# Kernel tuning notes

Hardware: AMD Instinct MI355X
Metric: run time of the kernel (lower is better)

## Reference

```python
import jax, jax.numpy as jnp
import numpy as np

N_NODES = 100000


def _degree_norms(src, dst, n):
    ones = jnp.ones(src.shape[0], dtype=jnp.float32)
    deg_out = jax.ops.segment_sum(ones, src, num_segments=n)
    deg_in = jax.ops.segment_sum(ones, dst, num_segments=n)
    norm_src = jnp.where(deg_out > 0, jax.lax.rsqrt(jnp.maximum(deg_out, 1.0)), 0.0)
    norm_dst = jnp.where(deg_in > 0, jax.lax.rsqrt(jnp.maximum(deg_in, 1.0)), 0.0)
    return norm_src, norm_dst


def _gcn_layer(x, W, b, src, dst, norm_src, norm_dst, n):
    # DGL GraphConv norm='both': D_dst^{-1/2} A D_src^{-1/2} X W + b
    h = (x * norm_src[:, None]) @ W          # [N, d_out]
    agg = jax.ops.segment_sum(h[src], dst, num_segments=n)  # SpMM gather/scatter
    return agg * norm_dst[:, None] + b


def setup_inputs() -> dict:
    key = jax.random.key(0)
    ks = jax.random.split(key, 8)
    E = 1600000
    x = jax.random.normal(ks[0], (N_NODES, 128), dtype=jnp.float32)
    edge_index = jax.random.randint(ks[1], (2, E), 0, N_NODES, dtype=jnp.int64)
    s = 1.0 / np.sqrt(128.0)
    W1 = jax.random.uniform(ks[2], (128, 128), jnp.float32, -s, s)
    b1 = jnp.zeros((128,), jnp.float32)
    W2 = jax.random.uniform(ks[3], (128, 128), jnp.float32, -s, s)
    b2 = jnp.zeros((128,), jnp.float32)
    W3 = jax.random.uniform(ks[4], (128, 256), jnp.float32, -s, s)
    b3 = jnp.zeros((256,), jnp.float32)
    return {"x": x, "edge_index": edge_index, "W1": W1, "b1": b1,
            "W2": W2, "b2": b2, "W3": W3, "b3": b3}


def reference(x, edge_index, W1, b1, W2, b2, W3, b3):
    src, dst = edge_index[0], edge_index[1]
    norm_src, norm_dst = _degree_norms(src, dst, N_NODES)
    h = jax.nn.relu(_gcn_layer(x, W1, b1, src, dst, norm_src, norm_dst, N_NODES))
    h = jax.nn.relu(_gcn_layer(h, W2, b2, src, dst, norm_src, norm_dst, N_NODES))
    h = _gcn_layer(h, W3, b3, src, dst, norm_src, norm_dst, N_NODES)
    return (h, edge_index)
```

## Files before the change

kernel.cpp:

```cpp
#include <hip/hip_runtime.h>

typedef _Float16 f16;
typedef _Float16 f16x8 __attribute__((ext_vector_type(8)));
typedef float f32x2 __attribute__((ext_vector_type(2)));
typedef float f32x4 __attribute__((ext_vector_type(4)));
typedef int i32x4 __attribute__((ext_vector_type(4)));

#define ROWB 1024
#define OFF_AGG 0
#define OFF_SA 256
#define OFF_SB 384
#define OFF_ADJ 768

__device__ __forceinline__ float bf2f(unsigned short h) {
  return __uint_as_float(((unsigned)h) << 16);
}
__device__ __forceinline__ unsigned short f2bf(float f) {
  unsigned u = __float_as_uint(f);
  u += 0x7fffu + ((u >> 16) & 1u);
  return (unsigned short)(u >> 16);
}
__device__ __forceinline__ float scrub(float v) {
  if (!(v == v)) return 0.f;
  return fminf(fmaxf(v, -65504.f), 65504.f);
}
__device__ __forceinline__ float scrub8(float v) {
  if (!(v == v)) return 0.f;
  return fminf(fmaxf(v, -240.f), 240.f);
}
__device__ __forceinline__ int iclamp(int v, int lo, int hi) {
  return v < lo ? lo : (v > hi ? hi : v);
}
__device__ __forceinline__ int adj_read(const char* H, int i) {
  return *(const int*)(H + ((size_t)(i >> 6)) * ROWB + OFF_ADJ + (i & 63) * 4);
}
__device__ __forceinline__ void adj_write(char* H, int i, int v) {
  *(int*)(H + ((size_t)(i >> 6)) * ROWB + OFF_ADJ + (i & 63) * 4) = v;
}
__device__ __forceinline__ int cread(const char* H, size_t base, int i) {
  return *(const int*)(H + base + ((size_t)(i >> 7)) * ROWB + (i & 127) * 4);
}
__device__ __forceinline__ i32x4 cread4(const char* H, size_t base, int i) {
  return *(const i32x4*)(H + base + ((size_t)(i >> 7)) * ROWB + (i & 127) * 4);
}
__device__ __forceinline__ void cwrite(char* H, size_t base, int i, int v) {
  *(int*)(H + base + ((size_t)(i >> 7)) * ROWB + (i & 127) * 4) = v;
}
__device__ __forceinline__ int2 pread(const char* H, size_t base, int i) {
  return *(const int2*)(H + base + ((size_t)(i >> 6)) * ROWB + (i & 63) * 8);
}
__device__ __forceinline__ void pwrite(char* H, size_t base, int i, int2 v) {
  *(int2*)(H + base + ((size_t)(i >> 6)) * ROWB + (i & 63) * 8) = v;
}
__device__ __forceinline__ int enc4(float a, float b, float c, float d) {
  int w = __builtin_amdgcn_cvt_pk_fp8_f32(a, b, 0, false);
  w = __builtin_amdgcn_cvt_pk_fp8_f32(c, d, w, true);
  return w;
}
__device__ __forceinline__ void dec_acc(i32x4 w, float* acc, float sc) {
#pragma unroll
  for (int d = 0; d < 4; ++d) {
    f32x2 lo = __builtin_amdgcn_cvt_pk_f32_fp8(w[d], false);
    f32x2 hi = __builtin_amdgcn_cvt_pk_f32_fp8(w[d], true);
    acc[d * 4 + 0] += sc * lo[0];
    acc[d * 4 + 1] += sc * lo[1];
    acc[d * 4 + 2] += sc * hi[0];
    acc[d * 4 + 3] += sc * hi[1];
  }
}

__global__ __launch_bounds__(64) void k_detect(const int* __restrict__ ei,
                                               int* __restrict__ flag) {
  int lane = threadIdx.x;
  int v = ei[2 * lane + 1];
  unsigned long long m = __ballot(v == 0);
  if (lane == 0) *flag = (m == 0xFFFFFFFFFFFFFFFFull) ? 1 : 0;
}

__global__ __launch_bounds__(256) void k_compact(const int* __restrict__ ei, int E,
                                                 int n, const int* __restrict__ flag,
                                                 char* __restrict__ H, size_t srcB,
                                                 size_t dstB, float* __restrict__ eout) {
  const int sh = *flag;
  const int tid = threadIdx.x;
  const int base = blockIdx.x * 1024 + tid;
  const int m = 2 * E;
#pragma unroll
  for (int k = 0; k < 4; ++k) {
    int i = base + k * 256;
    if (i < m) {
      int v = ei[(size_t)i << sh];
      eout[i] = bf2f(f2bf((float)v));
      int c = iclamp(v, 0, n - 1);
      if (i < E) cwrite(H, srcB, i, c);
      else cwrite(H, dstB, i - E, c);
    }
  }
}

__global__ __launch_bounds__(256) void k_coarse(char* __restrict__ H, size_t dstB,
                                                size_t cB, int E, int R, int CE) {
  __shared__ unsigned c[64];
  const int tid = threadIdx.x;
  if (tid < 64) c[tid] = 0;
  __syncthreads();
  const int lo = blockIdx.x * CE, hi = min(lo + CE, E);
  for (int i = lo + tid; i < hi; i += 256) {
    unsigned d = (unsigned)cread(H, dstB, i);
    atomicAdd(&c[d / (unsigned)R], 1u);
  }
  __syncthreads();
  if (tid < 64) cwrite(H, cB, tid * 256 + (int)blockIdx.x, (int)c[tid]);
}

__global__ __launch_bounds__(1024) void k_cscan(char* __restrict__ H, size_t cB) {
  __shared__ int bs[1024];
  const int tid = threadIdx.x;
  const int per = 16;
  const int base = tid * per;
  int vals[16];
  int sum = 0;
#pragma unroll
  for (int j = 0; j < per; ++j) {
    vals[j] = cread(H, cB, base + j);
    sum += vals[j];
  }
  bs[tid] = sum;
  __syncthreads();
  for (int off = 1; off < 1024; off <<= 1) {
    int t = (tid >= off) ? bs[tid - off] : 0;
    __syncthreads();
    bs[tid] += t;
    __syncthreads();
  }
  int ex = bs[tid] - sum;
#pragma unroll
  for (int j = 0; j < per; ++j) {
    int v = vals[j];
    cwrite(H, cB, base + j, ex);
    ex += v;
  }
}

__global__ __launch_bounds__(256) void k_bucket(char* __restrict__ H, size_t srcB,
                                                size_t dstB, size_t cB, size_t pB,
                                                int E, int R, int CE) {
  __shared__ int cu[64];
  const int tid = threadIdx.x;
  if (tid < 64) cu[tid] = cread(H, cB, tid * 256 + (int)blockIdx.x);
  __syncthreads();
  const int lo = blockIdx.x * CE, hi = min(lo + CE, E);
  for (int i = lo + tid; i < hi; i += 256) {
    int s = cread(H, srcB, i);
    int d = cread(H, dstB, i);
    int pos = atomicAdd(&cu[(unsigned)d / (unsigned)R], 1);
    pwrite(H, pB, pos, make_int2(s, d));
  }
}

__global__ __launch_bounds__(512) void k_hsrc(char* __restrict__ H, size_t srcB,
                                              size_t poB, int NPAD, int n, int E, int R) {
  extern __shared__ unsigned hh[];
  const int r = blockIdx.x >> 2, sl = blockIdx.x & 3;
  const int lo = r * R;
  if (lo >= n) return;
  const int hi = min(lo + R, n);
  const int tid = threadIdx.x;
  for (int j = tid; j < R; j += 512) hh[j] = 0;
  __syncthreads();
  int ES = (((E + 3) / 4) + 3) & ~3;
  const int s0 = sl * ES, s1 = min(s0 + ES, E);
  const int span = (unsigned)(hi - lo);
  const int m4 = s0 + ((s1 - s0) & ~3);
  for (int i = s0 + tid * 4; i < m4; i += 2048) {
    i32x4 v = cread4(H, srcB, i);
#pragma unroll
    for (int k = 0; k < 4; ++k) {
      unsigned u = (unsigned)(v[k] - lo);
      if (u < (unsigned)span) atomicAdd(&hh[u], 1u);
    }
  }
  for (int i = m4 + tid; i < s1; i += 512) {
    unsigned u = (unsigned)(cread(H, srcB, i) - lo);
    if (u < (unsigned)span) atomicAdd(&hh[u], 1u);
  }
  __syncthreads();
  for (int j = tid; j < hi - lo; j += 512) cwrite(H, poB, sl * NPAD + lo + j, (int)hh[j]);
}

__global__ __launch_bounds__(1024) void k_hdst(char* __restrict__ H, size_t pB,
                                               size_t cB, unsigned* __restrict__ degi,
                                               int n, int E, int R) {
  extern __shared__ unsigned hh2[];
  const int r = blockIdx.x;
  const int lo = r * R;
  if (lo >= n) return;
  const int hi = min(lo + R, n);
  const int tid = threadIdx.x;
  for (int j = tid; j < R; j += 1024) hh2[j] = 0;
  __syncthreads();
  const int b0 = cread(H, cB, r * 256);
  const int b1 = (r == (int)gridDim.x - 1) ? E : cread(H, cB, (r + 1) * 256);
  for (int i = b0 + tid; i < b1; i += 1024) {
    int2 p = pread(H, pB, i);
    unsigned u = (unsigned)(p.y - lo);
    if (u < (unsigned)(hi - lo)) atomicAdd(&hh2[u], 1u);
  }
  __syncthreads();
  for (int j = tid; j < hi - lo; j += 1024) degi[lo + j] = hh2[j];
}

__global__ __launch_bounds__(256) void k_scan1(const int* __restrict__ deg, int n,
                                               int* __restrict__ bsum) {
  __shared__ int sh[256];
  int tid = threadIdx.x;
  int i = blockIdx.x * 256 + tid;
  sh[tid] = (i < n) ? deg[i] : 0;
  __syncthreads();
  for (int s = 128; s > 0; s >>= 1) {
    if (tid < s) sh[tid] += sh[tid + s];
    __syncthreads();
  }
  if (tid == 0) bsum[blockIdx.x] = sh[0];
}

__global__ __launch_bounds__(512) void k_scan2(int* __restrict__ bsum, int nb,
                                               int* __restrict__ total_out) {
  __shared__ int sh[512];
  int tid = threadIdx.x;
  int v = (tid < nb) ? bsum[tid] : 0;
  sh[tid] = v;
  __syncthreads();
  for (int off = 1; off < 512; off <<= 1) {
    int t = (tid >= off) ? sh[tid - off] : 0;
    __syncthreads();
    sh[tid] += t;
    __syncthreads();
  }
  if (tid < nb) bsum[tid] = sh[tid] - v;
  if (tid == 0) *total_out = sh[511];
}

__global__ __launch_bounds__(256) void k_scan3(const int* __restrict__ deg,
                                               const int* __restrict__ bsum,
                                               int* __restrict__ rowptr, int n) {
  __shared__ int sh[256];
  int tid = threadIdx.x;
  int i = blockIdx.x * 256 + tid;
  int v = (i < n) ? deg[i] : 0;
  sh[tid] = v;
  __syncthreads();
  for (int off = 1; off < 256; off <<= 1) {
    int t = (tid >= off) ? sh[tid - off] : 0;
    __syncthreads();
    sh[tid] += t;
    __syncthreads();
  }
  if (i < n) rowptr[i] = bsum[blockIdx.x] + sh[tid] - v;
}

__global__ __launch_bounds__(1024) void k_fillp(char* __restrict__ H, size_t pB,
                                                size_t cB, const int* __restrict__ rowptr,
                                                int n, int E, int R, int CAP) {
  extern __shared__ int sm[];
  int* cur = sm;
  int* stg = sm + R;
  const int r = blockIdx.x;
  const int lo = r * R;
  if (lo >= n) return;
  const int hi = min(lo + R, n);
  const int tid = threadIdx.x;
  const int segBase = rowptr[lo];
  const int segEnd = rowptr[hi];
  for (int j = tid; j < hi - lo; j += 1024) cur[j] = rowptr[lo + j] - segBase;
  __syncthreads();
  const int b0 = cread(H, cB, r * 256);
  const int b1 = (r == (int)gridDim.x - 1) ? E : cread(H, cB, (r + 1) * 256);
  for (int i = b0 + tid; i < b1; i += 1024) {
    int2 p = pread(H, pB, i);
    unsigned u = (unsigned)(p.y - lo);
    if (u < (unsigned)(hi - lo)) {
      int slot = atomicAdd(&cur[u], 1);
      if (slot < CAP) stg[slot] = p.x;
      else adj_write(H, iclamp(segBase + slot, 0, E - 1), p.x);
    }
  }
  __syncthreads();
  int m = segEnd - segBase;
  if (m > CAP) m = CAP;
  for (int j = tid; j < m; j += 1024) adj_write(H, segBase + j, stg[j]);
}

__global__ __launch_bounds__(256) void k_normscale(char* __restrict__ H, size_t poB,
                                                   int NPAD, unsigned* __restrict__ dego,
                                                   unsigned* __restrict__ degi,
                                                   const float* __restrict__ X, int n) {
  __shared__ float ns[256];
  const int tid = threadIdx.x;
  const int rb = blockIdx.x * 256;
  int r = rb + tid;
  float f = 0.f;
  if (r < n) {
    unsigned a = 0;
#pragma unroll
    for (int s = 0; s < 4; ++s) a += (unsigned)cread(H, poB, s * NPAD + r);
    f = a ? rsqrtf((float)a) : 0.f;
    dego[r] = __float_as_uint(f);
    unsigned b = degi[r];
    degi[r] = __float_as_uint(b ? rsqrtf((float)b) : 0.f);
  }
  ns[tid] = f;
  __syncthreads();
  const int nrow = (n - rb < 256) ? (n - rb) : 256;
  for (int q = tid; q < nrow * 32; q += 256) {
    int lr = q >> 5, c = q & 31;
    int row = rb + lr;
    float4 v = ((const float4*)X)[(size_t)row * 32 + c];
    float s = ns[lr];
    int w = enc4(scrub8(v.x * s), scrub8(v.y * s), scrub8(v.z * s), scrub8(v.w * s));
    *(int*)(H + (size_t)row * ROWB + OFF_SB + c * 4) = w;
  }
}

__global__ __launch_bounds__(256) void k_aggregate(const char* __restrict__ H,
                                                   int sinOff,
                                                   const int* __restrict__ rowptr,
                                                   const unsigned* __restrict__ ndst,
                                                   int n, int E) {
  const int wv = blockIdx.x * 4 + (threadIdx.x >> 6);
  const int lane = threadIdx.x & 63;
  const int gw0 = wv * 2, gw1 = gw0 + 1;
  if (gw0 >= n) return;
  int s0 = iclamp(rowptr[gw0], 0, E);
  int e0 = iclamp(rowptr[gw0 + 1], s0, E);
  const bool has1 = (gw1 < n);
  int s1 = has1 ? iclamp(rowptr[gw1], 0, E) : 0;
  int e1 = has1 ? iclamp(rowptr[gw1 + 1], s1, E) : 0;
  const char* Sin = H + sinOff;
  const int grp = lane >> 3;
  const int sub = lane & 7;
  float a0[16] = {}, a1[16] = {};
  int i0 = s0, i1 = s1;
  while (i0 + 8 <= e0 && i1 + 8 <= e1) {
    int nA = iclamp(adj_read(H, i0 + grp), 0, n - 1);
    int nB = iclamp(adj_read(H, i1 + grp), 0, n - 1);
    i32x4 wA = *(const i32x4*)(Sin + (size_t)nA * ROWB + sub * 16);
    i32x4 wB = *(const i32x4*)(Sin + (size_t)nB * ROWB + sub * 16);
    dec_acc(wA, a0, 1.f);
    dec_acc(wB, a1, 1.f);
    i0 += 8;
    i1 += 8;
  }
  for (; i0 + 8 <= e0; i0 += 8) {
    int nA = iclamp(adj_read(H, i0 + grp), 0, n - 1);
    i32x4 wA = *(const i32x4*)(Sin + (size_t)nA * ROWB + sub * 16);
    dec_acc(wA, a0, 1.f);
  }
  for (; i1 + 8 <= e1; i1 += 8) {
    int nB = iclamp(adj_read(H, i1 + grp), 0, n - 1);
    i32x4 wB = *(const i32x4*)(Sin + (size_t)nB * ROWB + sub * 16);
    dec_acc(wB, a1, 1.f);
  }
  for (; i0 < e0; i0 += 8) {
    int idx = i0 + grp;
    float sc = (idx < e0) ? 1.f : 0.f;
    int nb = iclamp(adj_read(H, idx < e0 ? idx : i0), 0, n - 1);
    i32x4 w = *(const i32x4*)(Sin + (size_t)nb * ROWB + sub * 16);
    dec_acc(w, a0, sc);
  }
  for (; i1 < e1; i1 += 8) {
    int idx = i1 + grp;
    float sc = (idx < e1) ? 1.f : 0.f;
    int nb = iclamp(adj_read(H, idx < e1 ? idx : i1), 0, n - 1);
    i32x4 w = *(const i32x4*)(Sin + (size_t)nb * ROWB + sub * 16);
    dec_acc(w, a1, sc);
  }
#pragma unroll
  for (int j = 0; j < 16; ++j) {
    a0[j] += __shfl_xor(a0[j], 8, 64);
    a0[j] += __shfl_xor(a0[j], 16, 64);
    a0[j] += __shfl_xor(a0[j], 32, 64);
    a1[j] += __shfl_xor(a1[j], 8, 64);
    a1[j] += __shfl_xor(a1[j], 16, 64);
    a1[j] += __shfl_xor(a1[j], 32, 64);
  }
  if (lane < 8) {
    float nd = __uint_as_float(ndst[gw0]);
    f16x8 o0, o1;
#pragma unroll
    for (int j = 0; j < 8; ++j) {
      o0[j] = (f16)scrub(a0[j] * nd);
      o1[j] = (f16)scrub(a0[8 + j] * nd);
    }
    char* dst = ((char*)H) + OFF_AGG + (size_t)gw0 * ROWB + lane * 32;
    *(f16x8*)dst = o0;
    *(f16x8*)(dst + 16) = o1;
  } else if (lane < 16 && has1) {
    int l = lane & 7;
    float nd = __uint_as_float(ndst[gw1]);
    f16x8 o0, o1;
#pragma unroll
    for (int j = 0; j < 8; ++j) {
      o0[j] = (f16)scrub(a1[j] * nd);
      o1[j] = (f16)scrub(a1[8 + j] * nd);
    }
    char* dst = ((char*)H) + OFF_AGG + (size_t)gw1 * ROWB + l * 32;
    *(f16x8*)dst = o0;
    *(f16x8*)(dst + 16) = o1;
  }
}

template <int DOUT, bool MID>
__global__ __launch_bounds__(256) void k_gemm(const char* __restrict__ A,
                                              const float* __restrict__ W,
                                              const float* __restrict__ bias,
                                              const unsigned* __restrict__ nsrc,
                                              char* __restrict__ OUT, int n) {
  extern __shared__ char smem_raw[];
  f16* sB = (f16*)smem_raw;
  float* sBias = (float*)(smem_raw + DOUT * 128 * 2);
  const int tid = threadIdx.x;
  for (int idx = tid; idx < 128 * DOUT; idx += 256) {
    int k = idx / DOUT;
    int nn = idx % DOUT;
    int g = (k >> 3) ^ (nn & 15);
    sB[nn * 128 + (g << 3) + (k & 7)] = (f16)scrub(W[idx]);
  }
  for (int idx = tid; idx < DOUT; idx += 256) sBias[idx] = bias[idx];
  __syncthreads();
  const int wave = tid >> 6, lane = tid & 63;
  const int quad = lane >> 4, l16 = lane & 15;
  const int rowbase = blockIdx.x * 128 + wave * 32;
  constexpr int NT = DOUT / 16;
  f32x4 acc[2][NT] = {};
  int r0 = rowbase + l16;      if (r0 > n - 1) r0 = n - 1;
  int r1 = rowbase + 16 + l16; if (r1 > n - 1) r1 = n - 1;
#pragma unroll
  for (int ks = 0; ks < 4; ++ks) {
    const int k0 = ks * 32 + quad * 8;
    const int kg = ks * 4 + quad;
    f16x8 a0 = *(const f16x8*)(A + (size_t)r0 * ROWB + k0 * 2);
    f16x8 a1 = *(const f16x8*)(A + (size_t)r1 * ROWB + k0 * 2);
#pragma unroll
    for (int nt = 0; nt < NT; ++nt) {
      int nn = nt * 16 + l16;
      f16x8 b = *(const f16x8*)(sB + nn * 128 + ((kg ^ l16) << 3));
      acc[0][nt] = __builtin_amdgcn_mfma_f32_16x16x32_f16(b, a0, acc[0][nt], 0, 0, 0);
      acc[1][nt] = __builtin_amdgcn_mfma_f32_16x16x32_f16(b, a1, acc[1][nt], 0, 0, 0);
    }
  }
#pragma unroll
  for (int mt = 0; mt < 2; ++mt) {
    const int row = rowbase + mt * 16 + l16;
    if (row >= n) continue;
    const float ns = MID ? __uint_as_float(nsrc[row]) : 1.f;
#pragma unroll
    for (int nt = 0; nt < NT; ++nt) {
      const int col0 = nt * 16 + quad * 4;
      f32x4 bv = *(const f32x4*)(sBias + col0);
      f32x4 v;
#pragma unroll
      for (int j = 0; j < 4; ++j) v[j] = acc[mt][nt][j] + bv[j];
      if (MID) {
        float o[4];
#pragma unroll
        for (int j = 0; j < 4; ++j) {
          float x = fminf(fmaxf(v[j], 0.f) * ns, 240.f);
          if (!(x == x)) x = 0.f;
          o[j] = x;
        }
        *(int*)(OUT + (size_t)row * ROWB + col0) = enc4(o[0], o[1], o[2], o[3]);
      } else {
#pragma unroll
        for (int j = 0; j < 4; ++j) v[j] = scrub(v[j]);
        *(f32x4*)(OUT + (size_t)row * ROWB + col0 * 4) = v;
      }
    }
  }
}

extern "C" void kernel_launch(void* const* d_in, const int* in_sizes, int n_in,
                              void* d_out, int out_size, void* d_ws, size_t ws_size,
                              hipStream_t stream) {
  const float* X = (const float*)d_in[0];
  const int* EI = (const int*)d_in[1];
  const float* W1 = (const float*)d_in[2];
  const float* B1 = (const float*)d_in[3];
  const float* W2 = (const float*)d_in[4];
  const float* B2 = (const float*)d_in[5];
  const float* W3 = (const float*)d_in[6];
  const float* B3 = (const float*)d_in[7];

  const int n = in_sizes[0] / 128;
  const int E = in_sizes[1] / 2;

  char* w = (char*)d_ws;
  const size_t nb = ((size_t)n * 4 + 1023) & ~(size_t)1023;
  int* flag        = (int*)(w);
  unsigned* dego   = (unsigned*)(w + 1024);
  unsigned* degi   = (unsigned*)(w + 1024 + nb);
  int* rowptr      = (int*)(w + 1024 + 2 * nb);
  int* bsum        = (int*)(w + 1024 + 3 * nb);

  char* H = (char*)d_out;

  const int kRows  = (E + 63) / 64;
  const int cR32   = (E + 127) / 128;
  const int pRows  = (E + 63) / 64;
  const int poRows = (n + 127) / 128;
  const int NPAD   = poRows * 128;
  const size_t srcB = (size_t)kRows * ROWB + 512;
  const size_t dstB = srcB + (size_t)cR32 * ROWB;
  const size_t pB   = dstB + (size_t)cR32 * ROWB;
  const size_t poB  = pB + (size_t)pRows * ROWB;
  const size_t cB   = poB + (size_t)4 * poRows * ROWB;

  const int R  = (n + 63) / 64;
  const int NR = 64;
  const int NB = 256;
  const int CE = (E + NB - 1) / NB;
  const int CAP = 28672;

  const int gc = (2 * E + 1023) / 1024;
  const int gN = (n + 255) / 256;
  const int g2 = (n + 7) / 8;
  const int gG = (n + 127) / 128;

  k_detect<<<1, 64, 0, stream>>>(EI, flag);
  k_compact<<<gc, 256, 0, stream>>>(EI, E, n, flag, H, srcB, dstB,
                                    (float*)d_out + (size_t)n * 256);
  k_coarse<<<NB, 256, 0, stream>>>(H, dstB, cB, E, R, CE);
  k_cscan<<<1, 1024, 0, stream>>>(H, cB);
  k_bucket<<<NB, 256, 0, stream>>>(H, srcB, dstB, cB, pB, E, R, CE);
  k_hsrc<<<NR * 4, 512, (size_t)R * 4, stream>>>(H, srcB, poB, NPAD, n, E, R);
  k_hdst<<<NR, 1024, (size_t)R * 4, stream>>>(H, pB, cB, degi, n, E, R);
  k_scan1<<<gN, 256, 0, stream>>>((const int*)degi, n, bsum);
  k_scan2<<<1, 512, 0, stream>>>(bsum, gN, rowptr + n);
  k_scan3<<<gN, 256, 0, stream>>>((const int*)degi, bsum, rowptr, n);
  k_fillp<<<NR, 1024, (size_t)(R + CAP) * 4, stream>>>(H, pB, cB, rowptr, n, E, R, CAP);
  k_normscale<<<gN, 256, 0, stream>>>(H, poB, NPAD, dego, degi, X, n);

  k_aggregate<<<g2, 256, 0, stream>>>(H, OFF_SB, rowptr, degi, n, E);
  k_gemm<128, true><<<gG, 256, 128 * 128 * 2 + 128 * 4, stream>>>(H + OFF_AGG, W1, B1,
                                                                  dego, H + OFF_SA, n);
  k_aggregate<<<g2, 256, 0, stream>>>(H, OFF_SA, rowptr, degi, n, E);
  k_gemm<128, true><<<gG, 256, 128 * 128 * 2 + 128 * 4, stream>>>(H + OFF_AGG, W2, B2,
                                                                  dego, H + OFF_SB, n);
  k_aggregate<<<g2, 256, 0, stream>>>(H, OFF_SB, rowptr, degi, n, E);
  k_gemm<256, false><<<gG, 256, 256 * 128 * 2 + 256 * 4, stream>>>(H + OFF_AGG, W3, B3,
                                                                   dego, H, n);
}
```

Before: 642.8 us.

## Repartition source-degree histogram into 8 range buckets by 24 edge slices

The out-degree histogram kernel now splits nodes into 8 ranges of about 12.5k instead of 64 ranges of about 1.6k. It also splits the edges into 24 slices instead of 4, so 192 blocks each read 1/24 of the edges rather than 256 blocks each reading 1/4. This is meant to cut the total redundant reads of the source array, which drop from 64x to 8x, at the cost of a larger shared histogram per block and 24 partial counts summed in normscale. Separately, the GEMM weight staging now loads W as float4 instead of scalar floats.

```diff
diff --git a/kernel.cpp b/kernel.cpp
--- a/kernel.cpp
+++ b/kernel.cpp
@@ -159,30 +159,31 @@
 }
 
 __global__ __launch_bounds__(512) void k_hsrc(char* __restrict__ H, size_t srcB,
-                                              size_t poB, int NPAD, int n, int E, int R) {
+                                              size_t poB, int NPAD, int n, int E,
+                                              int RS, int NS) {
   extern __shared__ unsigned hh[];
-  const int r = blockIdx.x >> 2, sl = blockIdx.x & 3;
-  const int lo = r * R;
+  const int r = blockIdx.x / NS, sl = blockIdx.x % NS;
+  const int lo = r * RS;
   if (lo >= n) return;
-  const int hi = min(lo + R, n);
-  const int tid = threadIdx.x;
-  for (int j = tid; j < R; j += 512) hh[j] = 0;
-  __syncthreads();
-  int ES = (((E + 3) / 4) + 3) & ~3;
+  const int hi = min(lo + RS, n);
+  const int tid = threadIdx.x;
+  for (int j = tid; j < RS; j += 512) hh[j] = 0;
+  __syncthreads();
+  int ES = (((E + NS - 1) / NS) + 3) & ~3;
   const int s0 = sl * ES, s1 = min(s0 + ES, E);
-  const int span = (unsigned)(hi - lo);
+  const unsigned span = (unsigned)(hi - lo);
   const int m4 = s0 + ((s1 - s0) & ~3);
   for (int i = s0 + tid * 4; i < m4; i += 2048) {
     i32x4 v = cread4(H, srcB, i);
 #pragma unroll
     for (int k = 0; k < 4; ++k) {
       unsigned u = (unsigned)(v[k] - lo);
-      if (u < (unsigned)span) atomicAdd(&hh[u], 1u);
+      if (u < span) atomicAdd(&hh[u], 1u);
     }
   }
   for (int i = m4 + tid; i < s1; i += 512) {
     unsigned u = (unsigned)(cread(H, srcB, i) - lo);
-    if (u < (unsigned)span) atomicAdd(&hh[u], 1u);
+    if (u < span) atomicAdd(&hh[u], 1u);
   }
   __syncthreads();
   for (int j = tid; j < hi - lo; j += 512) cwrite(H, poB, sl * NPAD + lo + j, (int)hh[j]);
@@ -292,7 +293,8 @@
 }
 
 __global__ __launch_bounds__(256) void k_normscale(char* __restrict__ H, size_t poB,
-                                                   int NPAD, unsigned* __restrict__ dego,
+                                                   int NPAD, int NS,
+                                                   unsigned* __restrict__ dego,
                                                    unsigned* __restrict__ degi,
                                                    const float* __restrict__ X, int n) {
   __shared__ float ns[256];
@@ -302,8 +304,7 @@
   float f = 0.f;
   if (r < n) {
     unsigned a = 0;
-#pragma unroll
-    for (int s = 0; s < 4; ++s) a += (unsigned)cread(H, poB, s * NPAD + r);
+    for (int s = 0; s < NS; ++s) a += (unsigned)cread(H, poB, s * NPAD + r);
     f = a ? rsqrtf((float)a) : 0.f;
     dego[r] = __float_as_uint(f);
     unsigned b = degi[r];
@@ -420,11 +421,16 @@
   f16* sB = (f16*)smem_raw;
   float* sBias = (float*)(smem_raw + DOUT * 128 * 2);
   const int tid = threadIdx.x;
-  for (int idx = tid; idx < 128 * DOUT; idx += 256) {
+  for (int idx = tid * 4; idx < 128 * DOUT; idx += 1024) {
+    float4 wv = *(const float4*)(W + idx);
     int k = idx / DOUT;
-    int nn = idx % DOUT;
-    int g = (k >> 3) ^ (nn & 15);
-    sB[nn * 128 + (g << 3) + (k & 7)] = (f16)scrub(W[idx]);
+    int nn0 = idx % DOUT;
+#pragma unroll
+    for (int j = 0; j < 4; ++j) {
+      int nn = nn0 + j;
+      int g = (k >> 3) ^ (nn & 15);
+      sB[nn * 128 + (g << 3) + (k & 7)] = (f16)scrub((&wv.x)[j]);
+    }
   }
   for (int idx = tid; idx < DOUT; idx += 256) sBias[idx] = bias[idx];
   __syncthreads();
@@ -509,17 +515,21 @@
   const int pRows  = (E + 63) / 64;
   const int poRows = (n + 127) / 128;
   const int NPAD   = poRows * 128;
+  const int NS     = 24;
   const size_t srcB = (size_t)kRows * ROWB + 512;
   const size_t dstB = srcB + (size_t)cR32 * ROWB;
   const size_t pB   = dstB + (size_t)cR32 * ROWB;
   const size_t poB  = pB + (size_t)pRows * ROWB;
-  const size_t cB   = poB + (size_t)4 * poRows * ROWB;
+  const size_t cB   = poB + (size_t)NS * poRows * ROWB;
 
   const int R  = (n + 63) / 64;
   const int NR = 64;
   const int NB = 256;
   const int CE = (E + NB - 1) / NB;
   const int CAP = 28672;
+
+  const int RS  = (n + 7) / 8;
+  const int NRS = 8;
 
   const int gc = (2 * E + 1023) / 1024;
   const int gN = (n + 255) / 256;
@@ -532,13 +542,13 @@
   k_coarse<<<NB, 256, 0, stream>>>(H, dstB, cB, E, R, CE);
   k_cscan<<<1, 1024, 0, stream>>>(H, cB);
   k_bucket<<<NB, 256, 0, stream>>>(H, srcB, dstB, cB, pB, E, R, CE);
-  k_hsrc<<<NR * 4, 512, (size_t)R * 4, stream>>>(H, srcB, poB, NPAD, n, E, R);
+  k_hsrc<<<NRS * NS, 512, (size_t)RS * 4, stream>>>(H, srcB, poB, NPAD, n, E, RS, NS);
   k_hdst<<<NR, 1024, (size_t)R * 4, stream>>>(H, pB, cB, degi, n, E, R);
   k_scan1<<<gN, 256, 0, stream>>>((const int*)degi, n, bsum);
   k_scan2<<<1, 512, 0, stream>>>(bsum, gN, rowptr + n);
   k_scan3<<<gN, 256, 0, stream>>>((const int*)degi, bsum, rowptr, n);
   k_fillp<<<NR, 1024, (size_t)(R + CAP) * 4, stream>>>(H, pB, cB, rowptr, n, E, R, CAP);
-  k_normscale<<<gN, 256, 0, stream>>>(H, poB, NPAD, dego, degi, X, n);
+  k_normscale<<<gN, 256, 0, stream>>>(H, poB, NPAD, NS, dego, degi, X, n);
 
   k_aggregate<<<g2, 256, 0, stream>>>(H, OFF_SB, rowptr, degi, n, E);
   k_gemm<128, true><<<gG, 256, 128 * 128 * 2 + 128 * 4, stream>>>(H + OFF_AGG, W1, B1,
```

Result: faster. 579.7 us (-9.8%).
